# Optimization experiments

Hardware: AMD Instinct MI355X
Metric: run time of the kernel (lower is better)

Reference implementation:

```python
import jax, jax.numpy as jnp
import numpy as np

N_NODES = 50000


def _add_self_loops(edge_index, n):
    loops = jnp.arange(n, dtype=edge_index.dtype)
    src = jnp.concatenate([edge_index[0], loops])
    dst = jnp.concatenate([edge_index[1], loops])
    return src, dst


def _gcn_norm(src, dst, n):
    # symmetric normalization deg^-1/2 (degrees include self-loops), as in PyG GCNConv
    ones = jnp.ones_like(dst, dtype=jnp.float32)
    deg = jax.ops.segment_sum(ones, dst, num_segments=n)
    dinv = jnp.where(deg > 0, jax.lax.rsqrt(deg), 0.0)
    return dinv[src] * dinv[dst]


def _gcn_conv(x, W, b, src, dst, norm, n):
    h = x @ W                                  # [N, d_out] dense transform first (d_out <= d_in)
    msg = h[src] * norm[:, None]               # gather + per-edge scale
    out = jax.ops.segment_sum(msg, dst, num_segments=n)  # scatter-add aggregation
    return out + b


def setup_inputs() -> dict:
    key = jax.random.key(0)
    ks = jax.random.split(key, 5)
    n, e = N_NODES, 1_600_000
    x = jax.random.normal(ks[0], (n, 512), dtype=jnp.float32)
    edge_index = jax.random.randint(ks[1], (2, e), 0, n, dtype=jnp.int64)
    def glorot(k, fi, fo):
        s = jnp.sqrt(6.0 / (fi + fo)).astype(jnp.float32)
        return jax.random.uniform(k, (fi, fo), jnp.float32, -s, s)
    return {
        "x": x,
        "edge_index": edge_index,
        "W0": glorot(ks[2], 512, 256), "b0": jnp.zeros((256,), jnp.float32),
        "W1": glorot(ks[3], 256, 256), "b1": jnp.zeros((256,), jnp.float32),
        "W2": glorot(ks[4], 256, 128), "b2": jnp.zeros((128,), jnp.float32),
    }


def reference(x, edge_index, W0, b0, W1, b1, W2, b2):
    n = x.shape[0]
    src, dst = _add_self_loops(edge_index, n)
    norm = _gcn_norm(src, dst, n)
    h = jax.nn.relu(_gcn_conv(x, W0, b0, src, dst, norm, n))
    h = jax.nn.relu(_gcn_conv(h, W1, b1, src, dst, norm, n))
    z = _gcn_conv(h, W2, b2, src, dst, norm, n)
    return z
```

## Files before the change

### kernel.cpp

```cpp
#include <hip/hip_runtime.h>
#include <hip/hip_bf16.h>
#include <type_traits>

#define NN 50000
#define CNT_S 16

typedef __attribute__((ext_vector_type(8))) short bf16x8;
typedef __attribute__((ext_vector_type(4))) float f32x4;
typedef unsigned int u32;

__device__ __forceinline__ ushort f2bf(float f) {
    unsigned u = __builtin_bit_cast(unsigned, f);
    unsigned r = (u + 0x7fffu + ((u >> 16) & 1u)) >> 16;
    return (ushort)r;
}
__device__ __forceinline__ float bflo(unsigned v) { return __builtin_bit_cast(float, v << 16); }
__device__ __forceinline__ float bfhi(unsigned v) { return __builtin_bit_cast(float, v & 0xffff0000u); }

__device__ __forceinline__ void gld16(const void* g, void* l) {
    __builtin_amdgcn_global_load_lds((const __attribute__((address_space(1))) u32*)g,
                                     (__attribute__((address_space(3))) u32*)l, 16, 0, 0);
}

__device__ __forceinline__ int load_idx(const void* ei, long long pos, int is64) {
    return is64 ? (int)(((const long long*)ei)[pos]) : ((const int*)ei)[pos];
}

__global__ void k_initw(int* cnt, int ncnt, const unsigned int* ei, int npairs, int* flag,
                        const float* __restrict__ W0, ushort* __restrict__ WT0,
                        const float* __restrict__ W1, ushort* __restrict__ WT1,
                        const float* __restrict__ W2, ushort* __restrict__ WT2,
                        const float* __restrict__ x, ushort* __restrict__ xbf,
                        long long n8, int nbi) {
    if ((int)blockIdx.x >= nbi) {
        long long id = (long long)(blockIdx.x - nbi) * 256 + threadIdx.x;
        if (id < n8) {
            const float* src = x + id * 8;
            float4 f0 = *(const float4*)src;
            float4 f1 = *(const float4*)(src + 4);
            ushort tmp[8] = {f2bf(f0.x), f2bf(f0.y), f2bf(f0.z), f2bf(f0.w),
                             f2bf(f1.x), f2bf(f1.y), f2bf(f1.z), f2bf(f1.w)};
            *(uint4*)&xbf[id * 8] = *(uint4*)tmp;
        }
        return;
    }
    int id = blockIdx.x * 256 + threadIdx.x;
    if (id < ncnt) cnt[id] = 0;
    if (blockIdx.x == 0) {
        __shared__ int any_nz;
        if (threadIdx.x == 0) any_nz = 0;
        __syncthreads();
        for (int p = threadIdx.x; p < npairs; p += blockDim.x) {
            if (ei[2 * p + 1] != 0u) atomicOr(&any_nz, 1);
        }
        __syncthreads();
        if (threadIdx.x == 0) *flag = (any_nz == 0) ? 1 : 0;
    }
    const float* W; ushort* WT; int K, N, loc;
    if (id < 131072)      { W = W0; WT = WT0; K = 512; N = 256; loc = id; }
    else if (id < 196608) { W = W1; WT = WT1; K = 256; N = 256; loc = id - 131072; }
    else if (id < 229376) { W = W2; WT = WT2; K = 256; N = 128; loc = id - 196608; }
    else return;
    int nn = loc / K, k = loc - nn * K;
    WT[loc] = f2bf(W[(long long)k * N + nn]);
}

#define LOFF(r, s) (((r) * 8 + ((s) ^ ((r) & 7))) * 8)

__device__ __forceinline__ void gemm_tile_u16(const ushort* __restrict__ A,
                                              const ushort* __restrict__ WT,
                                              ushort* __restrict__ C,
                                              int M, int N, int K, int m0, int n0,
                                              ushort* As, ushort* Bs) {
    int t = threadIdx.x;
    int lane = t & 63;
    int w = t >> 6;
    int wr = (w >> 1) * 64, wc = (w & 1) * 64;
    f32x4 acc[4][4] = {};
    for (int k0 = 0; k0 < K; k0 += 64) {
#pragma unroll
        for (int j = 0; j < 4; ++j) {
            int id = (w * 4 + j) * 64 + lane;
            int r = id >> 3, sp = id & 7;
            int s = sp ^ (r & 7);
            gld16(WT + (long long)(n0 + r) * K + k0 + s * 8, &Bs[(r * 8 + sp) * 8]);
        }
#pragma unroll
        for (int j = 0; j < 4; ++j) {
            int rbase = (w * 4 + j) * 8;
            if (m0 + rbase < M) {
                int id = rbase * 8 + lane;
                int r = id >> 3, sp = id & 7;
                int s = sp ^ (r & 7);
                gld16(A + (long long)(m0 + r) * K + k0 + s * 8, &As[(r * 8 + sp) * 8]);
            }
        }
        __syncthreads();
#pragma unroll
        for (int kk = 0; kk < 2; ++kk) {
            int ks = kk * 4 + (lane >> 4);
            bf16x8 a[4], b[4];
#pragma unroll
            for (int m = 0; m < 4; ++m)
                a[m] = *(bf16x8*)&As[LOFF(wr + m * 16 + (lane & 15), ks)];
#pragma unroll
            for (int nn = 0; nn < 4; ++nn)
                b[nn] = *(bf16x8*)&Bs[LOFF(wc + nn * 16 + (lane & 15), ks)];
#pragma unroll
            for (int m = 0; m < 4; ++m)
#pragma unroll
                for (int nn = 0; nn < 4; ++nn)
                    acc[m][nn] = __builtin_amdgcn_mfma_f32_16x16x32_bf16(a[m], b[nn], acc[m][nn], 0, 0, 0);
        }
        __syncthreads();
    }
#pragma unroll
    for (int m = 0; m < 4; ++m) {
#pragma unroll
        for (int i = 0; i < 4; ++i) {
            int row = m0 + wr + m * 16 + (lane >> 4) * 4 + i;
            if (row < M) {
#pragma unroll
                for (int nn = 0; nn < 4; ++nn) {
                    int col = n0 + wc + nn * 16 + (lane & 15);
                    C[(long long)row * N + col] = f2bf(acc[m][nn][i]);
                }
            }
        }
    }
}

__global__ __launch_bounds__(256) void k_countg(const void* ei, long long E,
                                                const int* __restrict__ flag,
                                                int* cnt, int* __restrict__ ord, int nbg,
                                                const ushort* __restrict__ A,
                                                const ushort* __restrict__ WT,
                                                ushort* __restrict__ C, int M, int N, int K) {
    __shared__ ushort As[8192];
    __shared__ ushort Bs[8192];
    if ((int)blockIdx.x < nbg) {
        int b = (int)blockIdx.x;
        gemm_tile_u16(A, WT, C, M, N, K, (b >> 1) * 128, (b & 1) * 128, As, Bs);
        return;
    }
    long long e = (long long)((int)blockIdx.x - nbg) * 256 + threadIdx.x;
    if (e < E) {
        int dst = load_idx(ei, E + e, *flag);
        ord[e] = atomicAdd(&cnt[(long long)dst * CNT_S], 1);
    }
}

__global__ void k_count(const void* ei, long long E, const int* flag,
                        int* cnt, int* __restrict__ ord) {
    long long e = (long long)blockIdx.x * blockDim.x + threadIdx.x;
    if (e < E) {
        int dst = load_idx(ei, E + e, *flag);
        ord[e] = atomicAdd(&cnt[(long long)dst * CNT_S], 1);
    }
}

__global__ __launch_bounds__(1024) void k_scan_a(const int* __restrict__ cnt,
                                                 int* __restrict__ bsum,
                                                 float* __restrict__ dinv, int n) {
    __shared__ int wsum[16];
    int i = blockIdx.x * 1024 + threadIdx.x;
    int lane = (int)threadIdx.x & 63, w = (int)threadIdx.x >> 6;
    int v = (i < n) ? cnt[(long long)i * CNT_S] : 0;
    int pv = (v + 7) & ~7;
    if (i < n) dinv[i] = rsqrtf((float)(v + 1));
    int s = pv;
#pragma unroll
    for (int off = 1; off < 64; off <<= 1) s += __shfl_xor(s, off);
    if (lane == 0) wsum[w] = s;
    __syncthreads();
    if (threadIdx.x == 0) {
        int t = 0;
#pragma unroll
        for (int k = 0; k < 16; ++k) t += wsum[k];
        bsum[blockIdx.x] = t;
    }
}

__global__ void k_scan_b(const int* __restrict__ bsum, int* __restrict__ bbase,
                         int* __restrict__ offs_n, int nb) {
    int lane = (int)threadIdx.x;
    int v = (lane < nb) ? bsum[lane] : 0;
    int x = v;
#pragma unroll
    for (int off = 1; off < 64; off <<= 1) {
        int y = __shfl_up(x, off);
        if (lane >= off) x += y;
    }
    if (lane < nb) bbase[lane] = x - v;
    if (lane == nb - 1) *offs_n = x;
}

__global__ __launch_bounds__(1024) void k_scan_c(const int* __restrict__ cnt,
                                                 const int* __restrict__ bbase,
                                                 int* __restrict__ offs,
                                                 int2* __restrict__ epk, int n) {
    __shared__ int wsum[16];
    int i = blockIdx.x * 1024 + threadIdx.x;
    int lane = (int)threadIdx.x & 63, w = (int)threadIdx.x >> 6;
    int v = (i < n) ? cnt[(long long)i * CNT_S] : 0;
    int pv = (v + 7) & ~7;
    int x = pv;
#pragma unroll
    for (int off = 1; off < 64; off <<= 1) {
        int y = __shfl_up(x, off);
        if (lane >= off) x += y;
    }
    if (lane == 63) wsum[w] = x;
    __syncthreads();
    if (w == 0) {
        int pvv = (lane < 16) ? wsum[lane] : 0;
#pragma unroll
        for (int off = 1; off < 16; off <<= 1) {
            int py = __shfl_up(pvv, off);
            if (lane >= off) pvv += py;
        }
        if (lane < 16) wsum[lane] = pvv;
    }
    __syncthreads();
    int wbase = (w > 0) ? wsum[w - 1] : 0;
    if (i < n) {
        int o = bbase[blockIdx.x] + wbase + x - pv;
        offs[i] = o;
        for (int j = o + v; j < o + pv; ++j) epk[j] = make_int2(0, 0);
    }
}

#define KE 8
__global__ void k_bucket(const void* ei, long long E, const int* __restrict__ flag,
                         const float* __restrict__ dinv, const int* __restrict__ offs,
                         const int* __restrict__ ord, int2* __restrict__ epk,
                         int n, int nchunk_e, int pn) {
    int p = blockIdx.x & 7;
    int c = blockIdx.x >> 3;
    int lo = p * pn;
    int hi = lo + pn; if (hi > n) hi = n;
    int is64 = *flag;
    long long base = (long long)c * (256 * KE) + threadIdx.x;
#pragma unroll
    for (int k = 0; k < KE; ++k) {
        long long e = base + k * 256;
        if (e < E) {
            int dst = load_idx(ei, E + e, is64);
            if (dst >= lo && dst < hi) {
                int src = load_idx(ei, e, is64);
                int pos = offs[dst] + ord[e];
                epk[pos] = make_int2(src, __builtin_bit_cast(int, dinv[src] * dinv[dst]));
            }
        }
    }
}

template <typename TA>
__global__ __launch_bounds__(256) void k_gemm_mfma(const TA* __restrict__ A,
                                                   const ushort* __restrict__ WT,
                                                   ushort* __restrict__ C,
                                                   int M, int N, int K) {
    __shared__ ushort As[8192];
    __shared__ ushort Bs[8192];
    int m0 = blockIdx.y * 128, n0 = blockIdx.x * 128;
    if constexpr (std::is_same<TA, float>::value) {
        int t = threadIdx.x;
        int lane = t & 63;
        int w = t >> 6;
        int wr = (w >> 1) * 64, wc = (w & 1) * 64;
        f32x4 acc[4][4] = {};
        for (int k0 = 0; k0 < K; k0 += 64) {
#pragma unroll
            for (int j = 0; j < 4; ++j) {
                int id = (w * 4 + j) * 64 + lane;
                int r = id >> 3, sp = id & 7;
                int s = sp ^ (r & 7);
                gld16(WT + (long long)(n0 + r) * K + k0 + s * 8, &Bs[(r * 8 + sp) * 8]);
            }
#pragma unroll
            for (int j = 0; j < 4; ++j) {
                int id = t + j * 256;
                int r = id >> 3, s = id & 7;
                int grow = m0 + r;
                if (grow < M) {
                    const float* src = A + (long long)grow * K + k0 + s * 8;
                    float4 f0 = *(const float4*)src;
                    float4 f1 = *(const float4*)(src + 4);
                    ushort tmp[8] = {f2bf(f0.x), f2bf(f0.y), f2bf(f0.z), f2bf(f0.w),
                                     f2bf(f1.x), f2bf(f1.y), f2bf(f1.z), f2bf(f1.w)};
                    *(uint4*)&As[LOFF(r, s)] = *(uint4*)tmp;
                }
            }
            __syncthreads();
#pragma unroll
            for (int kk = 0; kk < 2; ++kk) {
                int ks = kk * 4 + (lane >> 4);
                bf16x8 a[4], b[4];
#pragma unroll
                for (int m = 0; m < 4; ++m)
                    a[m] = *(bf16x8*)&As[LOFF(wr + m * 16 + (lane & 15), ks)];
#pragma unroll
                for (int nn = 0; nn < 4; ++nn)
                    b[nn] = *(bf16x8*)&Bs[LOFF(wc + nn * 16 + (lane & 15), ks)];
#pragma unroll
                for (int m = 0; m < 4; ++m)
#pragma unroll
                    for (int nn = 0; nn < 4; ++nn)
                        acc[m][nn] = __builtin_amdgcn_mfma_f32_16x16x32_bf16(a[m], b[nn], acc[m][nn], 0, 0, 0);
            }
            __syncthreads();
        }
#pragma unroll
        for (int m = 0; m < 4; ++m) {
#pragma unroll
            for (int i = 0; i < 4; ++i) {
                int row = m0 + wr + m * 16 + (lane >> 4) * 4 + i;
                if (row < M) {
#pragma unroll
                    for (int nn = 0; nn < 4; ++nn) {
                        int col = n0 + wc + nn * 16 + (lane & 15);
                        C[(long long)row * N + col] = f2bf(acc[m][nn][i]);
                    }
                }
            }
        }
    } else {
        gemm_tile_u16(A, WT, C, M, N, K, m0, n0, As, Bs);
    }
}

template <int DT, bool RELU, bool OUTF32>
__global__ __launch_bounds__(128) void k_aggs(const ushort* __restrict__ h,
                                              const int* __restrict__ offs,
                                              const int2* __restrict__ epk,
                                              const float* __restrict__ dinv,
                                              const float* __restrict__ bias,
                                              void* __restrict__ outp, int n, int foff) {
    int node = __builtin_amdgcn_readfirstlane((int)(blockIdx.x * 2 + (threadIdx.x >> 6)));
    if (node >= n) return;
    int t = (int)threadIdx.x & 63;
    float di = dinv[node];
    float dii = di * di;

    unsigned v0 = *(const unsigned*)&h[(long long)node * DT + foff + t * 2];
    float2 bs = *(const float2*)&bias[foff + t * 2];
    float a0 = bs.x + dii * bflo(v0);
    float a1 = bs.y + dii * bfhi(v0);

    int s = offs[node], e = offs[node + 1];

    for (int j = s; j < e; j += 8) {
        int2 p[8];
#pragma unroll
        for (int u = 0; u < 8; ++u) p[u] = epk[j + u];
        unsigned v[8];
#pragma unroll
        for (int u = 0; u < 8; ++u)
            v[u] = *(const unsigned*)&h[(long long)p[u].x * DT + foff + t * 2];
#pragma unroll
        for (int u = 0; u < 8; ++u) {
            float wgt = __builtin_bit_cast(float, p[u].y);
            a0 += wgt * bflo(v[u]);
            a1 += wgt * bfhi(v[u]);
        }
    }

    if (RELU) { a0 = fmaxf(a0, 0.f); a1 = fmaxf(a1, 0.f); }
    long long oidx = ((long long)node * DT + foff) / 2 + t;
    if constexpr (OUTF32) {
        ((float2*)outp)[oidx] = make_float2(a0, a1);
    } else {
        unsigned pk = (unsigned)f2bf(a0) | ((unsigned)f2bf(a1) << 16);
        ((unsigned*)outp)[oidx] = pk;
    }
}

extern "C" void kernel_launch(void* const* d_in, const int* in_sizes, int n_in,
                              void* d_out, int out_size, void* d_ws, size_t ws_size,
                              hipStream_t stream) {
    const float* x  = (const float*)d_in[0];
    const void*  ei = d_in[1];
    const float* W0 = (const float*)d_in[2];
    const float* b0 = (const float*)d_in[3];
    const float* W1 = (const float*)d_in[4];
    const float* b1 = (const float*)d_in[5];
    const float* W2 = (const float*)d_in[6];
    const float* b2 = (const float*)d_in[7];
    float* out = (float*)d_out;

    const int n = NN;
    const long long E = (long long)in_sizes[1] / 2;
    const int ncnt = n * CNT_S;
    const int nbscan = (n + 1023) / 1024;

    char* ws = (char*)d_ws;
    int*    cnt  = (int*)(ws);
    int*    offs = (int*)(ws + 3400 * 1024);
    float*  dinv = (float*)(ws + 3700 * 1024);
    int*    flag = (int*)(ws + 3960 * 1024);
    int*    bsum = (int*)(ws + 3964 * 1024);
    int*    bbase= (int*)(ws + 3968 * 1024);
    int2*   epk  = (int2*)(ws + 4ll * 1024 * 1024);
    ushort* WT0  = (ushort*)(ws + 20ll * 1024 * 1024);
    ushort* WT1  = (ushort*)(ws + 20ll * 1024 * 1024 + 512 * 1024);
    ushort* WT2  = (ushort*)(ws + 20ll * 1024 * 1024 + 768 * 1024);
    ushort* hA   = (ushort*)(ws + 21ll * 1024 * 1024);
    ushort* hB   = (ushort*)(ws + 47ll * 1024 * 1024);
    ushort* xbf  = (ushort*)(ws + 73ll * 1024 * 1024);
    int*    ord  = (int*)hB;
    const size_t need_xbf = 73ll * 1024 * 1024 + 51200000ll;
    const bool have_xbf = (ws_size >= need_xbf);

    const int nbi = (ncnt + 255) / 256;
    const long long n8 = (long long)n * 512 / 8;
    const int nbx = have_xbf ? (int)((n8 + 255) / 256) : 0;

    k_initw<<<nbi + nbx, 256, 0, stream>>>(cnt, ncnt, (const unsigned int*)ei, 4096, flag,
                                           W0, WT0, W1, WT1, W2, WT2, x, xbf, n8, nbi);

    int mt = (n + 127) / 128;
    int nb2 = (n + 1) / 2;
    const int nbc = (int)((E + 255) / 256);

    if (have_xbf) {
        k_countg<<<2 * mt + nbc, 256, 0, stream>>>(ei, E, flag, cnt, ord, 2 * mt,
                                                   xbf, WT0, hA, n, 256, 512);
    } else {
        k_count<<<nbc, 256, 0, stream>>>(ei, E, flag, cnt, ord);
        k_gemm_mfma<float><<<dim3(2, mt), 256, 0, stream>>>(x, WT0, hA, n, 256, 512);
    }
    k_scan_a<<<nbscan, 1024, 0, stream>>>(cnt, bsum, dinv, n);
    k_scan_b<<<1, 64, 0, stream>>>(bsum, bbase, &offs[n], nbscan);
    k_scan_c<<<nbscan, 1024, 0, stream>>>(cnt, bbase, offs, epk, n);
    {
        int nchunk_e = (int)((E + 256 * KE - 1) / (256 * KE));
        int pn = (n + 7) / 8;
        k_bucket<<<8 * nchunk_e, 256, 0, stream>>>(
            ei, E, flag, dinv, offs, ord, epk, n, nchunk_e, pn);
    }

    k_aggs<256, true, false><<<nb2, 128, 0, stream>>>(hA, offs, epk, dinv, b0, hB, n, 0);
    k_aggs<256, true, false><<<nb2, 128, 0, stream>>>(hA, offs, epk, dinv, b0, hB, n, 128);

    k_gemm_mfma<ushort><<<dim3(2, mt), 256, 0, stream>>>(hB, WT1, hA, n, 256, 256);
    k_aggs<256, true, false><<<nb2, 128, 0, stream>>>(hA, offs, epk, dinv, b1, hB, n, 0);
    k_aggs<256, true, false><<<nb2, 128, 0, stream>>>(hA, offs, epk, dinv, b1, hB, n, 128);

    k_gemm_mfma<ushort><<<dim3(1, mt), 256, 0, stream>>>(hB, WT2, hA, n, 128, 256);
    k_aggs<128, false, true><<<nb2, 128, 0, stream>>>(hA, offs, epk, dinv, b2, out, n, 0);
}
```

Before: 442.5 us.

## Sub-bucket CSR edges by source range to improve gather locality

The per-destination counters, formerly padded to 16 slots with only one used, now hold 13 sub-bins keyed by source-node range (src>>12), and a per-node prefix over the sub-bins gives each edge a slot within its destination row. Edges in each CSR row therefore come out roughly sorted by source, which should give the aggregation kernels' gathers of h[src] better cache locality across rows. The count blocks are also moved ahead of the GEMM blocks in the fused launch. This costs an extra src load in counting, extra offs2 writes in the scan kernels, and a workspace layout change that overlays offs2 on hB.

```diff
diff --git a/kernel.cpp b/kernel.cpp
--- a/kernel.cpp
+++ b/kernel.cpp
@@ -3,7 +3,9 @@
 #include <type_traits>
 
 #define NN 50000
-#define CNT_S 16
+#define NT_SHIFT 12
+#define NT 13
+#define NB 16
 
 typedef __attribute__((ext_vector_type(8))) short bf16x8;
 typedef __attribute__((ext_vector_type(4))) float f32x4;
@@ -26,7 +28,7 @@
     return is64 ? (int)(((const long long*)ei)[pos]) : ((const int*)ei)[pos];
 }
 
-__global__ void k_initw(int* cnt, int ncnt, const unsigned int* ei, int npairs, int* flag,
+__global__ void k_initw(int* cnt2, int ncnt, const unsigned int* ei, int npairs, int* flag,
                         const float* __restrict__ W0, ushort* __restrict__ WT0,
                         const float* __restrict__ W1, ushort* __restrict__ WT1,
                         const float* __restrict__ W2, ushort* __restrict__ WT2,
@@ -45,7 +47,7 @@
         return;
     }
     int id = blockIdx.x * 256 + threadIdx.x;
-    if (id < ncnt) cnt[id] = 0;
+    if (id < ncnt) cnt2[id] = 0;
     if (blockIdx.x == 0) {
         __shared__ int any_nz;
         if (threadIdx.x == 0) any_nz = 0;
@@ -132,42 +134,62 @@
 
 __global__ __launch_bounds__(256) void k_countg(const void* ei, long long E,
                                                 const int* __restrict__ flag,
-                                                int* cnt, int* __restrict__ ord, int nbg,
+                                                int* cnt2, int* __restrict__ ord, int nbc,
                                                 const ushort* __restrict__ A,
                                                 const ushort* __restrict__ WT,
                                                 ushort* __restrict__ C, int M, int N, int K) {
     __shared__ ushort As[8192];
     __shared__ ushort Bs[8192];
-    if ((int)blockIdx.x < nbg) {
-        int b = (int)blockIdx.x;
-        gemm_tile_u16(A, WT, C, M, N, K, (b >> 1) * 128, (b & 1) * 128, As, Bs);
+    if ((int)blockIdx.x < nbc) {
+        long long e = (long long)blockIdx.x * 256 + threadIdx.x;
+        if (e < E) {
+            int is64 = *flag;
+            int dst = load_idx(ei, E + e, is64);
+            int src = load_idx(ei, e, is64);
+            int bin = (dst << 4) + (src >> NT_SHIFT);
+            ord[e] = atomicAdd(&cnt2[bin], 1);
+        }
         return;
     }
-    long long e = (long long)((int)blockIdx.x - nbg) * 256 + threadIdx.x;
-    if (e < E) {
-        int dst = load_idx(ei, E + e, *flag);
-        ord[e] = atomicAdd(&cnt[(long long)dst * CNT_S], 1);
-    }
+    int b = (int)blockIdx.x - nbc;
+    gemm_tile_u16(A, WT, C, M, N, K, (b >> 1) * 128, (b & 1) * 128, As, Bs);
 }
 
 __global__ void k_count(const void* ei, long long E, const int* flag,
-                        int* cnt, int* __restrict__ ord) {
+                        int* cnt2, int* __restrict__ ord) {
     long long e = (long long)blockIdx.x * blockDim.x + threadIdx.x;
     if (e < E) {
-        int dst = load_idx(ei, E + e, *flag);
-        ord[e] = atomicAdd(&cnt[(long long)dst * CNT_S], 1);
-    }
-}
-
-__global__ __launch_bounds__(1024) void k_scan_a(const int* __restrict__ cnt,
+        int is64 = *flag;
+        int dst = load_idx(ei, E + e, is64);
+        int src = load_idx(ei, e, is64);
+        int bin = (dst << 4) + (src >> NT_SHIFT);
+        ord[e] = atomicAdd(&cnt2[bin], 1);
+    }
+}
+
+__global__ __launch_bounds__(1024) void k_scan_a(const int* __restrict__ cnt2,
+                                                 int* __restrict__ offs2,
+                                                 int* __restrict__ cnt,
                                                  int* __restrict__ bsum,
                                                  float* __restrict__ dinv, int n) {
     __shared__ int wsum[16];
     int i = blockIdx.x * 1024 + threadIdx.x;
     int lane = (int)threadIdx.x & 63, w = (int)threadIdx.x >> 6;
-    int v = (i < n) ? cnt[(long long)i * CNT_S] : 0;
+    int v = 0;
+    if (i < n) {
+        int base = i * NB;
+        int acc = 0;
+#pragma unroll
+        for (int t = 0; t < NT; ++t) {
+            int c = cnt2[base + t];
+            offs2[base + t] = acc;
+            acc += c;
+        }
+        v = acc;
+        cnt[i] = v;
+        dinv[i] = rsqrtf((float)(v + 1));
+    }
     int pv = (v + 7) & ~7;
-    if (i < n) dinv[i] = rsqrtf((float)(v + 1));
     int s = pv;
 #pragma unroll
     for (int off = 1; off < 64; off <<= 1) s += __shfl_xor(s, off);
@@ -198,11 +220,12 @@
 __global__ __launch_bounds__(1024) void k_scan_c(const int* __restrict__ cnt,
                                                  const int* __restrict__ bbase,
                                                  int* __restrict__ offs,
+                                                 int* __restrict__ offs2,
                                                  int2* __restrict__ epk, int n) {
     __shared__ int wsum[16];
     int i = blockIdx.x * 1024 + threadIdx.x;
     int lane = (int)threadIdx.x & 63, w = (int)threadIdx.x >> 6;
-    int v = (i < n) ? cnt[(long long)i * CNT_S] : 0;
+    int v = (i < n) ? cnt[i] : 0;
     int pv = (v + 7) & ~7;
     int x = pv;
 #pragma unroll
@@ -226,13 +249,16 @@
     if (i < n) {
         int o = bbase[blockIdx.x] + wbase + x - pv;
         offs[i] = o;
+#pragma unroll
+        for (int t = 0; t < NT; ++t) offs2[i * NB + t] += o;
         for (int j = o + v; j < o + pv; ++j) epk[j] = make_int2(0, 0);
     }
 }
 
 #define KE 8
 __global__ void k_bucket(const void* ei, long long E, const int* __restrict__ flag,
-                         const float* __restrict__ dinv, const int* __restrict__ offs,
+                         const float* __restrict__ dinv,
+                         const int* __restrict__ offs2,
                          const int* __restrict__ ord, int2* __restrict__ epk,
                          int n, int nchunk_e, int pn) {
     int p = blockIdx.x & 7;
@@ -248,7 +274,7 @@
             int dst = load_idx(ei, E + e, is64);
             if (dst >= lo && dst < hi) {
                 int src = load_idx(ei, e, is64);
-                int pos = offs[dst] + ord[e];
+                int pos = offs2[(dst << 4) + (src >> NT_SHIFT)] + ord[e];
                 epk[pos] = make_int2(src, __builtin_bit_cast(int, dinv[src] * dinv[dst]));
             }
         }
@@ -390,17 +416,18 @@
 
     const int n = NN;
     const long long E = (long long)in_sizes[1] / 2;
-    const int ncnt = n * CNT_S;
+    const int ncnt = n * NB;
     const int nbscan = (n + 1023) / 1024;
 
     char* ws = (char*)d_ws;
-    int*    cnt  = (int*)(ws);
-    int*    offs = (int*)(ws + 3400 * 1024);
-    float*  dinv = (float*)(ws + 3700 * 1024);
-    int*    flag = (int*)(ws + 3960 * 1024);
-    int*    bsum = (int*)(ws + 3964 * 1024);
-    int*    bbase= (int*)(ws + 3968 * 1024);
-    int2*   epk  = (int2*)(ws + 4ll * 1024 * 1024);
+    int*    cnt2 = (int*)(ws);
+    int*    cnt  = (int*)(ws + 3300 * 1024);
+    int*    offs = (int*)(ws + 3550 * 1024);
+    float*  dinv = (float*)(ws + 3800 * 1024);
+    int*    flag = (int*)(ws + 4080 * 1024);
+    int*    bsum = (int*)(ws + 4084 * 1024);
+    int*    bbase= (int*)(ws + 4088 * 1024);
+    int2*   epk  = (int2*)(ws + 4100 * 1024);
     ushort* WT0  = (ushort*)(ws + 20ll * 1024 * 1024);
     ushort* WT1  = (ushort*)(ws + 20ll * 1024 * 1024 + 512 * 1024);
     ushort* WT2  = (ushort*)(ws + 20ll * 1024 * 1024 + 768 * 1024);
@@ -408,6 +435,7 @@
     ushort* hB   = (ushort*)(ws + 47ll * 1024 * 1024);
     ushort* xbf  = (ushort*)(ws + 73ll * 1024 * 1024);
     int*    ord  = (int*)hB;
+    int*    offs2= (int*)((char*)hB + 7ll * 1024 * 1024);
     const size_t need_xbf = 73ll * 1024 * 1024 + 51200000ll;
     const bool have_xbf = (ws_size >= need_xbf);
 
@@ -415,7 +443,7 @@
     const long long n8 = (long long)n * 512 / 8;
     const int nbx = have_xbf ? (int)((n8 + 255) / 256) : 0;
 
-    k_initw<<<nbi + nbx, 256, 0, stream>>>(cnt, ncnt, (const unsigned int*)ei, 4096, flag,
+    k_initw<<<nbi + nbx, 256, 0, stream>>>(cnt2, ncnt, (const unsigned int*)ei, 4096, flag,
                                            W0, WT0, W1, WT1, W2, WT2, x, xbf, n8, nbi);
 
     int mt = (n + 127) / 128;
@@ -423,20 +451,20 @@
     const int nbc = (int)((E + 255) / 256);
 
     if (have_xbf) {
-        k_countg<<<2 * mt + nbc, 256, 0, stream>>>(ei, E, flag, cnt, ord, 2 * mt,
+        k_countg<<<nbc + 2 * mt, 256, 0, stream>>>(ei, E, flag, cnt2, ord, nbc,
                                                    xbf, WT0, hA, n, 256, 512);
     } else {
-        k_count<<<nbc, 256, 0, stream>>>(ei, E, flag, cnt, ord);
+        k_count<<<nbc, 256, 0, stream>>>(ei, E, flag, cnt2, ord);
         k_gemm_mfma<float><<<dim3(2, mt), 256, 0, stream>>>(x, WT0, hA, n, 256, 512);
     }
-    k_scan_a<<<nbscan, 1024, 0, stream>>>(cnt, bsum, dinv, n);
+    k_scan_a<<<nbscan, 1024, 0, stream>>>(cnt2, offs2, cnt, bsum, dinv, n);
     k_scan_b<<<1, 64, 0, stream>>>(bsum, bbase, &offs[n], nbscan);
-    k_scan_c<<<nbscan, 1024, 0, stream>>>(cnt, bbase, offs, epk, n);
+    k_scan_c<<<nbscan, 1024, 0, stream>>>(cnt, bbase, offs, offs2, epk, n);
     {
         int nchunk_e = (int)((E + 256 * KE - 1) / (256 * KE));
         int pn = (n + 7) / 8;
         k_bucket<<<8 * nchunk_e, 256, 0, stream>>>(
-            ei, E, flag, dinv, offs, ord, epk, n, nchunk_e, pn);
+            ei, E, flag, dinv, offs2, ord, epk, n, nchunk_e, pn);
     }
 
     k_aggs<256, true, false><<<nb2, 128, 0, stream>>>(hA, offs, epk, dinv, b0, hB, n, 0);
```

Result: no change. 449.9 us (+1.7%).
